# Optimization experiments

Measured on AMD Instinct MI355X. Metric: run time of the kernel, lower is better.

## Reference

```python
import jax, jax.numpy as jnp
import numpy as np

N_HEADS = 16
D_MODEL = 1024
D_HEAD = D_MODEL // N_HEADS


def setup_inputs() -> dict:
    key = jax.random.key(0)
    k1, k2, k3 = jax.random.split(key, 3)
    b, t, d = 2, 2048, D_MODEL
    x = jax.random.normal(k1, (b, t, d), dtype=jnp.float32)
    # Linear weights stored as [in, out] so y = x @ W (equivalent to torch's x @ W.T)
    w_qkv = jax.random.normal(k2, (d, 3 * d), dtype=jnp.float32) * (1.0 / np.sqrt(d))
    w_out = jax.random.normal(k3, (d, d), dtype=jnp.float32) * (1.0 / np.sqrt(d))
    return {"x": x, "w_qkv": w_qkv, "w_out": w_out}


def reference(x, w_qkv, w_out):
    b, t, d = x.shape
    h, dh = N_HEADS, D_HEAD
    qkv = x @ w_qkv                                   # (b, t, 3d)
    q, k, v = jnp.split(qkv, 3, axis=-1)
    # (b, h, t, dh)
    q = q.reshape(b, t, h, dh).transpose(0, 2, 1, 3)
    k = k.reshape(b, t, h, dh).transpose(0, 2, 1, 3)
    v = v.reshape(b, t, h, dh).transpose(0, 2, 1, 3)
    scale = 1.0 / np.sqrt(dh).astype(np.float32)
    att = jnp.einsum('bhqd,bhkd->bhqk', q, k) * scale  # (b, h, t, t)
    causal = jnp.tril(jnp.ones((t, t), dtype=bool))
    att = jnp.where(causal, att, -jnp.inf)
    att = jax.nn.softmax(att, axis=-1)
    y = jnp.einsum('bhqk,bhkd->bhqd', att, v)          # (b, h, t, dh)
    y = y.transpose(0, 2, 1, 3).reshape(b, t, d)
    return y @ w_out
```

## Files before the change

### kernel.cpp

```cpp
#include <hip/hip_runtime.h>
#include <hip/hip_bf16.h>
#include <stdint.h>

typedef __bf16 bf16x8 __attribute__((ext_vector_type(8)));
typedef float  f32x4  __attribute__((ext_vector_type(4)));

#define B_   2
#define T_   2048
#define H_   16
#define DH_  64
#define DM_  1024
#define BH_  (B_*H_)
#define M_   (B_*T_)

#define QSCALE 0.18033688f
#define FIXED_M 8.0f

static __device__ __forceinline__ void gload_lds16(const void* g, void* lds) {
  __builtin_amdgcn_global_load_lds(
      (const __attribute__((address_space(1))) void*)(uintptr_t)g,
      (__attribute__((address_space(3))) void*)(uint32_t)(uintptr_t)lds,
      16, 0, 0);
}

__global__ void k_prep(const float* __restrict__ x, const float* __restrict__ wqkv,
                       const float* __restrict__ wout, __hip_bfloat16* __restrict__ xb,
                       __hip_bfloat16* __restrict__ wqkvT, __hip_bfloat16* __restrict__ woutT) {
  __shared__ float tile[32][33];
  const int bid = blockIdx.x, tid = threadIdx.x;
  if (bid < 4096) {
    int i = bid * 256 + tid;
    float4 v = reinterpret_cast<const float4*>(x)[i];
    alignas(8) __hip_bfloat16 t[4] = {__float2bfloat16(v.x), __float2bfloat16(v.y),
                                      __float2bfloat16(v.z), __float2bfloat16(v.w)};
    reinterpret_cast<uint2*>(xb)[i] = *reinterpret_cast<const uint2*>(t);
    return;
  }
  const float* in; __hip_bfloat16* out; int K, N, n0, k0;
  if (bid < 7168) {
    int t = bid - 4096; in = wqkv; out = wqkvT; K = 1024; N = 3072;
    n0 = (t % 96) * 32; k0 = (t / 96) * 32;
  } else {
    int t = bid - 7168; in = wout; out = woutT; K = 1024; N = 1024;
    n0 = (t % 32) * 32; k0 = (t / 32) * 32;
  }
  int kl = tid >> 3, n4 = (tid & 7) * 4;
  float4 v = *reinterpret_cast<const float4*>(in + (size_t)(k0 + kl) * N + n0 + n4);
  tile[kl][n4 + 0] = v.x; tile[kl][n4 + 1] = v.y; tile[kl][n4 + 2] = v.z; tile[kl][n4 + 3] = v.w;
  __syncthreads();
  int nl = tid >> 3, k4 = (tid & 7) * 4;
  alignas(8) __hip_bfloat16 t[4];
  #pragma unroll
  for (int j = 0; j < 4; ++j) t[j] = __float2bfloat16(tile[k4 + j][nl]);
  *reinterpret_cast<uint2*>(out + (size_t)(n0 + nl) * K + k0 + k4) = *reinterpret_cast<const uint2*>(t);
}

template<int BM, int BN, int FM, int FN>
static __device__ __forceinline__ void gemm_core_pipe(
    const __hip_bfloat16* __restrict__ A, const __hip_bfloat16* __restrict__ BT,
    int K, int brow, int bcol, __hip_bfloat16* As, __hip_bfloat16* Bs,
    f32x4 acc[FM][FN]) {
  constexpr int WGN = BN / (16 * FN);
  constexpr int LOADS = BM / 64 + BN / 64;
  constexpr int ASLOT = BM * 32, BSLOT = BN * 32;
  const int tid = threadIdx.x, wave = tid >> 6, lane = tid & 63;
  const int wr = wave / WGN, wc = wave % WGN;
  const int llo = lane & 15, lhi = lane >> 4;
  const int nk = K / 32;
  const int schunk = (lane & 3) ^ ((lane >> 3) & 3);
  auto stage = [&](int ks, int slot) {
    #pragma unroll
    for (int c = wave; c < BM / 16; c += 4)
      gload_lds16(A + (size_t)(brow + c * 16 + (lane >> 2)) * K + ks * 32 + schunk * 8,
                  As + slot * ASLOT + c * 512);
    #pragma unroll
    for (int c = wave; c < BN / 16; c += 4)
      gload_lds16(BT + (size_t)(bcol + c * 16 + (lane >> 2)) * K + ks * 32 + schunk * 8,
                  Bs + slot * BSLOT + c * 512);
  };
  stage(0, 0);
  stage(1, 1);
  const int rchunk = lhi ^ ((llo >> 1) & 3);
  for (int ks = 0; ks < nk; ++ks) {
    if constexpr (LOADS == 4)      asm volatile("s_waitcnt vmcnt(4)" ::: "memory");
    else if constexpr (LOADS == 3) asm volatile("s_waitcnt vmcnt(3)" ::: "memory");
    else                           asm volatile("s_waitcnt vmcnt(0)" ::: "memory");
    __builtin_amdgcn_sched_barrier(0);
    __builtin_amdgcn_s_barrier();
    __builtin_amdgcn_sched_barrier(0);
    const int s2 = (ks + 2 < nk) ? ks + 2 : nk - 1;
    stage(s2, (ks + 2) % 3);
    const __hip_bfloat16* Asl = As + (ks % 3) * ASLOT;
    const __hip_bfloat16* Bsl = Bs + (ks % 3) * BSLOT;
    bf16x8 a[FM], b[FN];
    #pragma unroll
    for (int i = 0; i < FM; ++i)
      a[i] = *reinterpret_cast<const bf16x8*>(
          Asl + (wr * FM * 16 + i * 16 + llo) * 32 + rchunk * 8);
    #pragma unroll
    for (int j = 0; j < FN; ++j)
      b[j] = *reinterpret_cast<const bf16x8*>(
          Bsl + (wc * FN * 16 + j * 16 + llo) * 32 + rchunk * 8);
    __builtin_amdgcn_s_setprio(1);
    #pragma unroll
    for (int i = 0; i < FM; ++i)
      #pragma unroll
      for (int j = 0; j < FN; ++j)
        acc[i][j] = __builtin_amdgcn_mfma_f32_16x16x32_bf16(a[i], b[j], acc[i][j], 0, 0, 0);
    __builtin_amdgcn_s_setprio(0);
  }
  asm volatile("s_waitcnt vmcnt(0)" ::: "memory");
}

__global__ __launch_bounds__(256) void k_gemm_qkv(
    const __hip_bfloat16* __restrict__ A, const __hip_bfloat16* __restrict__ BT,
    __hip_bfloat16* __restrict__ q_ws, __hip_bfloat16* __restrict__ k_ws,
    __hip_bfloat16* __restrict__ vT) {
  alignas(16) __shared__ __hip_bfloat16 As[3 * 128 * 32];
  alignas(16) __shared__ __hip_bfloat16 Bs[3 * 128 * 32];
  f32x4 acc[4][4] = {};
  const int brow = blockIdx.y * 128, bcol = blockIdx.x * 128;
  gemm_core_pipe<128, 128, 4, 4>(A, BT, DM_, brow, bcol, As, Bs, acc);
  const int tid = threadIdx.x, wave = tid >> 6, lane = tid & 63;
  const int wr = wave >> 1, wc = wave & 1;
  const int llo = lane & 15, lhi = lane >> 4;
  #pragma unroll
  for (int i = 0; i < 4; ++i) {
    const int tbase = brow + wr * 64 + i * 16 + lhi * 4;
    const int b = tbase >> 11, t = tbase & 2047;
    #pragma unroll
    for (int j = 0; j < 4; ++j) {
      int n = bcol + wc * 64 + j * 16 + llo;
      int part = n >> 10, rem = n & 1023, hh = rem >> 6, dh = rem & 63;
      if (part == 2) {
        alignas(8) __hip_bfloat16 tv[4];
        #pragma unroll
        for (int r = 0; r < 4; ++r) tv[r] = __float2bfloat16(acc[i][j][r]);
        *reinterpret_cast<uint2*>(
            vT + (((size_t)(b * H_ + hh)) * DH_ + dh) * T_ + t) =
            *reinterpret_cast<const uint2*>(tv);
      } else {
        float sc = (part == 0) ? QSCALE : 1.0f;
        __hip_bfloat16* dst = (part == 0) ? q_ws : k_ws;
        #pragma unroll
        for (int r = 0; r < 4; ++r)
          dst[(((size_t)(b * H_ + hh)) * T_ + t + r) * DH_ + dh] =
              __float2bfloat16(acc[i][j][r] * sc);
      }
    }
  }
}

__global__ __launch_bounds__(256) void k_gemm_out(
    const __hip_bfloat16* __restrict__ A, const __hip_bfloat16* __restrict__ BT,
    float* __restrict__ C) {
  alignas(16) __shared__ __hip_bfloat16 As[3 * 128 * 32];
  alignas(16) __shared__ __hip_bfloat16 Bs[3 * 64 * 32];
  f32x4 acc[4][2] = {};
  const int brow = blockIdx.y * 128, bcol = blockIdx.x * 64;
  gemm_core_pipe<128, 64, 4, 2>(A, BT, DM_, brow, bcol, As, Bs, acc);
  const int tid = threadIdx.x, wave = tid >> 6, lane = tid & 63;
  const int wr = wave >> 1, wc = wave & 1;
  const int llo = lane & 15, lhi = lane >> 4;
  #pragma unroll
  for (int i = 0; i < 4; ++i)
    #pragma unroll
    for (int j = 0; j < 2; ++j) {
      int n = bcol + wc * 32 + j * 16 + llo;
      #pragma unroll
      for (int r = 0; r < 4; ++r) {
        int m = brow + wr * 64 + i * 16 + lhi * 4 + r;
        C[(size_t)m * DM_ + n] = acc[i][j][r];
      }
    }
}

__global__ __launch_bounds__(512) void k_attn(
    const __hip_bfloat16* __restrict__ Q, const __hip_bfloat16* __restrict__ Kk,
    const __hip_bfloat16* __restrict__ VT, __hip_bfloat16* __restrict__ Y) {
  alignas(16) __shared__ __hip_bfloat16 Ks[4][64 * 64];
  alignas(16) __shared__ __hip_bfloat16 Vs[4][64 * 64];
  alignas(16) __shared__ __hip_bfloat16 Ps[8][16 * 64];
  const int bh = blockIdx.y;
  const int p  = blockIdx.x;
  const int tid = threadIdx.x, wave = tid >> 6, lane = tid & 63;
  const int llo = lane & 15, lhi = lane >> 4;
  const int qt   = (wave < 4) ? (31 - p) : p;
  const int myNt = qt + 1;
  const int ntA  = 32 - p;
  const int q0 = qt * 64;
  const int qbase = q0 + (wave & 3) * 16;
  const int myq = qbase + llo;

  const __hip_bfloat16* kb = Kk + (size_t)bh * T_ * DH_;
  const __hip_bfloat16* vb = VT + (size_t)bh * DH_ * T_;

  const int srow = lane >> 3;
  const int schunk = (lane & 7) ^ srow;
  const int rb = wave * 8;

  bf16x8 aq[2];
  #pragma unroll
  for (int k0 = 0; k0 < 2; ++k0)
    aq[k0] = *reinterpret_cast<const bf16x8*>(
        Q + ((size_t)bh * T_ + myq) * DH_ + k0 * 32 + lhi * 8);

  float lsum = 0.f;
  f32x4 o[4] = {};

  gload_lds16(kb + (size_t)(rb + srow) * DH_ + schunk * 8, &Ks[0][rb * 64]);
  gload_lds16(vb + (size_t)(rb + srow) * T_ + schunk * 8, &Vs[0][rb * 64]);
  gload_lds16(kb + (size_t)(64 + rb + srow) * DH_ + schunk * 8, &Ks[1][rb * 64]);
  gload_lds16(vb + (size_t)(rb + srow) * T_ + 64 + schunk * 8, &Vs[1][rb * 64]);

  char* psw = reinterpret_cast<char*>(&Ps[wave][0]);

  for (int it = 0; it < ntA; ++it) {
    const int cur = it & 3;
    {
      const int ts = (it + 2 < ntA) ? (it + 2) : (ntA - 1);
      const int bs = (it + 2) & 3;
      const int tn = ts * 64;
      gload_lds16(kb + (size_t)(tn + rb + srow) * DH_ + schunk * 8, &Ks[bs][rb * 64]);
      gload_lds16(vb + (size_t)(rb + srow) * T_ + tn + schunk * 8, &Vs[bs][rb * 64]);
    }
    asm volatile("s_waitcnt vmcnt(4)" ::: "memory");
    __builtin_amdgcn_sched_barrier(0);
    __builtin_amdgcn_s_barrier();
    __builtin_amdgcn_sched_barrier(0);

    if (it < myNt) {
      const __hip_bfloat16* ksb = Ks[cur];
      const __hip_bfloat16* vsb = Vs[cur];

      f32x4 s[4];
      __builtin_amdgcn_s_setprio(1);
      #pragma unroll
      for (int jn = 0; jn < 4; ++jn) {
        const __hip_bfloat16* krow = ksb + (jn * 16 + llo) * 64;
        bf16x8 b0 = *reinterpret_cast<const bf16x8*>(krow + ((lhi ^ (llo & 7)) << 3));
        bf16x8 b1 = *reinterpret_cast<const bf16x8*>(krow + (((4 + lhi) ^ (llo & 7)) << 3));
        f32x4 z = {};
        z = __builtin_amdgcn_mfma_f32_16x16x32_bf16(b0, aq[0], z, 0, 0, 0);
        z = __builtin_amdgcn_mfma_f32_16x16x32_bf16(b1, aq[1], z, 0, 0, 0);
        s[jn] = z;
      }
      __builtin_amdgcn_s_setprio(0);
      if (it == myNt - 1) {
        #pragma unroll
        for (int jn = 0; jn < 4; ++jn)
          #pragma unroll
          for (int r = 0; r < 4; ++r) {
            int tprime = q0 + jn * 16 + lhi * 4 + r;
            if (tprime > myq) s[jn][r] = -INFINITY;
          }
      }
      #pragma unroll
      for (int jn = 0; jn < 4; ++jn) {
        float p0 = __builtin_amdgcn_exp2f(s[jn][0] - FIXED_M);
        float p1 = __builtin_amdgcn_exp2f(s[jn][1] - FIXED_M);
        float p2 = __builtin_amdgcn_exp2f(s[jn][2] - FIXED_M);
        float p3 = __builtin_amdgcn_exp2f(s[jn][3] - FIXED_M);
        lsum += (p0 + p1) + (p2 + p3);
        alignas(8) __hip_bfloat16 hp[4] = {
            __float2bfloat16(p0), __float2bfloat16(p1),
            __float2bfloat16(p2), __float2bfloat16(p3)};
        int wbyte = llo * 128 + ((((jn << 1) | (lhi >> 1)) ^ (llo & 7)) << 4) + ((lhi & 1) << 3);
        *reinterpret_cast<uint2*>(psw + wbyte) = *reinterpret_cast<const uint2*>(hp);
      }
      asm volatile("" ::: "memory");
      bf16x8 ap0 = *reinterpret_cast<const bf16x8*>(
          &Ps[wave][llo * 64 + ((lhi ^ (llo & 7)) << 3)]);
      bf16x8 ap1 = *reinterpret_cast<const bf16x8*>(
          &Ps[wave][llo * 64 + (((4 + lhi) ^ (llo & 7)) << 3)]);
      __builtin_amdgcn_s_setprio(1);
      #pragma unroll
      for (int jd = 0; jd < 4; ++jd) {
        const __hip_bfloat16* vrow = vsb + (jd * 16 + llo) * 64;
        bf16x8 v0 = *reinterpret_cast<const bf16x8*>(vrow + ((lhi ^ (llo & 7)) << 3));
        bf16x8 v1 = *reinterpret_cast<const bf16x8*>(vrow + (((4 + lhi) ^ (llo & 7)) << 3));
        o[jd] = __builtin_amdgcn_mfma_f32_16x16x32_bf16(v0, ap0, o[jd], 0, 0, 0);
        o[jd] = __builtin_amdgcn_mfma_f32_16x16x32_bf16(v1, ap1, o[jd], 0, 0, 0);
      }
      __builtin_amdgcn_s_setprio(0);
    }
  }

  lsum += __shfl_xor(lsum, 16);
  lsum += __shfl_xor(lsum, 32);
  const float inv = 1.0f / lsum;

  const int b = bh >> 4, h = bh & 15;
  __hip_bfloat16* yrow = Y + ((size_t)(b * T_ + myq)) * DM_ + h * 64;
  #pragma unroll
  for (int jd = 0; jd < 4; ++jd) {
    alignas(8) __hip_bfloat16 t4[4];
    #pragma unroll
    for (int r = 0; r < 4; ++r) t4[r] = __float2bfloat16(o[jd][r] * inv);
    *reinterpret_cast<uint2*>(yrow + jd * 16 + lhi * 4) =
        *reinterpret_cast<const uint2*>(t4);
  }
}

extern "C" void kernel_launch(void* const* d_in, const int* in_sizes, int n_in,
                              void* d_out, int out_size, void* d_ws, size_t ws_size,
                              hipStream_t stream) {
  const float* x     = (const float*)d_in[0];
  const float* w_qkv = (const float*)d_in[1];
  const float* w_out = (const float*)d_in[2];
  float* out = (float*)d_out;
  char* ws = (char*)d_ws;

  size_t off = 0;
  __hip_bfloat16* xb    = (__hip_bfloat16*)(ws + off); off += (size_t)M_ * DM_ * 2;
  __hip_bfloat16* wqkvT = (__hip_bfloat16*)(ws + off); off += (size_t)3 * DM_ * DM_ * 2;
  __hip_bfloat16* woutT = (__hip_bfloat16*)(ws + off); off += (size_t)DM_ * DM_ * 2;
  __hip_bfloat16* q_ws  = (__hip_bfloat16*)(ws + off); off += (size_t)M_ * DM_ * 2;
  __hip_bfloat16* k_ws  = (__hip_bfloat16*)(ws + off); off += (size_t)M_ * DM_ * 2;
  __hip_bfloat16* vT    = (__hip_bfloat16*)(ws + off); off += (size_t)M_ * DM_ * 2;
  __hip_bfloat16* y_ws  = (__hip_bfloat16*)(ws + off); off += (size_t)M_ * DM_ * 2;
  (void)ws_size; (void)in_sizes; (void)n_in; (void)out_size;

  k_prep<<<8192, 256, 0, stream>>>(x, w_qkv, w_out, xb, wqkvT, woutT);

  k_gemm_qkv<<<dim3(3 * DM_ / 128, M_ / 128), 256, 0, stream>>>(xb, wqkvT, q_ws, k_ws, vT);

  k_attn<<<dim3(T_ / 128, BH_), 512, 0, stream>>>(q_ws, k_ws, vT, y_ws);

  k_gemm_out<<<dim3(DM_ / 64, M_ / 128), 256, 0, stream>>>(y_ws, woutT, out);
}
```

Before: 99.88 us.

## Rewrite QKV GEMM with 256x256 tiles, 8 waves, and double-buffered K=64 stages

Replaces the 128x128, 4-wave triple-buffered QKV projection GEMM with a 256x256 tile computed by 8 waves (512 threads). Each K step is 64 wide, double-buffered in LDS with an XOR swizzle, and split into four sub-phases that interleave the next-tile loads with MFMA work. The goal is more reuse per LDS byte and fewer global loads per FLOP. In exchange it uses 128 KB of LDS per block, adds extra barriers per sub-phase, and launches only 192 blocks, which may underfill the GPU's compute units.

```diff
diff --git a/kernel.cpp b/kernel.cpp
--- a/kernel.cpp
+++ b/kernel.cpp
@@ -15,6 +15,8 @@
 
 #define QSCALE 0.18033688f
 #define FIXED_M 8.0f
+
+#define SBAR() __builtin_amdgcn_sched_barrier(0)
 
 static __device__ __forceinline__ void gload_lds16(const void* g, void* lds) {
   __builtin_amdgcn_global_load_lds(
@@ -85,9 +87,9 @@
     if constexpr (LOADS == 4)      asm volatile("s_waitcnt vmcnt(4)" ::: "memory");
     else if constexpr (LOADS == 3) asm volatile("s_waitcnt vmcnt(3)" ::: "memory");
     else                           asm volatile("s_waitcnt vmcnt(0)" ::: "memory");
-    __builtin_amdgcn_sched_barrier(0);
+    SBAR();
     __builtin_amdgcn_s_barrier();
-    __builtin_amdgcn_sched_barrier(0);
+    SBAR();
     const int s2 = (ks + 2 < nk) ? ks + 2 : nk - 1;
     stage(s2, (ks + 2) % 3);
     const __hip_bfloat16* Asl = As + (ks % 3) * ASLOT;
@@ -112,25 +114,97 @@
   asm volatile("s_waitcnt vmcnt(0)" ::: "memory");
 }
 
-__global__ __launch_bounds__(256) void k_gemm_qkv(
+__global__ __launch_bounds__(512) void k_gemm_qkv(
     const __hip_bfloat16* __restrict__ A, const __hip_bfloat16* __restrict__ BT,
     __hip_bfloat16* __restrict__ q_ws, __hip_bfloat16* __restrict__ k_ws,
     __hip_bfloat16* __restrict__ vT) {
-  alignas(16) __shared__ __hip_bfloat16 As[3 * 128 * 32];
-  alignas(16) __shared__ __hip_bfloat16 Bs[3 * 128 * 32];
-  f32x4 acc[4][4] = {};
-  const int brow = blockIdx.y * 128, bcol = blockIdx.x * 128;
-  gemm_core_pipe<128, 128, 4, 4>(A, BT, DM_, brow, bcol, As, Bs, acc);
+  alignas(16) __shared__ __hip_bfloat16 Adb[2][256 * 64];
+  alignas(16) __shared__ __hip_bfloat16 Bdb[2][256 * 64];
   const int tid = threadIdx.x, wave = tid >> 6, lane = tid & 63;
-  const int wr = wave >> 1, wc = wave & 1;
   const int llo = lane & 15, lhi = lane >> 4;
+  const int wr = wave >> 2, wcn = wave & 3;
+  const int bcol = blockIdx.x * 256, brow = blockIdx.y * 256;
+
+  f32x4 acc[8][4] = {};
+
+  auto stageHalf = [&](const __hip_bfloat16* P, int baseRow, int ktS, int half,
+                       __hip_bfloat16* tile) {
+    #pragma unroll
+    for (int l = 0; l < 2; ++l) {
+      const int idxb = l * 512 + wave * 64;
+      const int rowt = half * 128 + (idxb >> 3) + (lane >> 3);
+      const int ch = lane & 7;
+      gload_lds16(P + (size_t)(baseRow + rowt) * DM_ + ktS * 64 + ((ch ^ (rowt & 7)) * 8),
+                  tile + half * (128 * 64) + idxb * 8);
+    }
+  };
+
+  stageHalf(A, brow, 0, 0, Adb[0]);
+  stageHalf(A, brow, 0, 1, Adb[0]);
+  stageHalf(BT, bcol, 0, 0, Bdb[0]);
+  stageHalf(BT, bcol, 0, 1, Bdb[0]);
+
+  for (int kt = 0; kt < 16; ++kt) {
+    const int buf = kt & 1;
+    const int bufn = buf ^ 1;
+    const int ktn = (kt < 15) ? kt + 1 : 15;
+    const __hip_bfloat16* At = Adb[buf];
+    const __hip_bfloat16* Bt = Bdb[buf];
+    #pragma unroll
+    for (int p = 0; p < 4; ++p) {
+      if (p == 0) {
+        stageHalf(A, brow, ktn, 0, Adb[bufn]);
+        stageHalf(A, brow, ktn, 1, Adb[bufn]);
+        asm volatile("s_waitcnt vmcnt(4)" ::: "memory");
+      } else if (p == 1) {
+        stageHalf(BT, bcol, ktn, 0, Bdb[bufn]);
+        stageHalf(BT, bcol, ktn, 1, Bdb[bufn]);
+      }
+      SBAR();
+      __builtin_amdgcn_s_barrier();
+      SBAR();
+      const int i0 = p >> 1, j0 = p & 1;
+      bf16x8 af[4][2], bfr[2][2];
+      #pragma unroll
+      for (int ii = 0; ii < 4; ++ii) {
+        const int rowt = wr * 128 + (i0 * 4 + ii) * 16 + llo;
+        #pragma unroll
+        for (int kk = 0; kk < 2; ++kk)
+          af[ii][kk] = *reinterpret_cast<const bf16x8*>(
+              At + rowt * 64 + (((kk * 4 + lhi) ^ (rowt & 7)) * 8));
+      }
+      #pragma unroll
+      for (int j2 = 0; j2 < 2; ++j2) {
+        const int rowb = wcn * 64 + (j0 * 2 + j2) * 16 + llo;
+        #pragma unroll
+        for (int kk = 0; kk < 2; ++kk)
+          bfr[j2][kk] = *reinterpret_cast<const bf16x8*>(
+              Bt + rowb * 64 + (((kk * 4 + lhi) ^ (rowb & 7)) * 8));
+      }
+      __builtin_amdgcn_s_setprio(1);
+      #pragma unroll
+      for (int ii = 0; ii < 4; ++ii)
+        #pragma unroll
+        for (int j2 = 0; j2 < 2; ++j2)
+          #pragma unroll
+          for (int kk = 0; kk < 2; ++kk)
+            acc[i0 * 4 + ii][j0 * 2 + j2] = __builtin_amdgcn_mfma_f32_16x16x32_bf16(
+                af[ii][kk], bfr[j2][kk], acc[i0 * 4 + ii][j0 * 2 + j2], 0, 0, 0);
+      __builtin_amdgcn_s_setprio(0);
+      SBAR();
+      __builtin_amdgcn_s_barrier();
+      SBAR();
+    }
+  }
+  asm volatile("s_waitcnt vmcnt(0)" ::: "memory");
+
   #pragma unroll
-  for (int i = 0; i < 4; ++i) {
-    const int tbase = brow + wr * 64 + i * 16 + lhi * 4;
+  for (int i = 0; i < 8; ++i) {
+    const int tbase = brow + wr * 128 + i * 16 + lhi * 4;
     const int b = tbase >> 11, t = tbase & 2047;
     #pragma unroll
     for (int j = 0; j < 4; ++j) {
-      int n = bcol + wc * 64 + j * 16 + llo;
+      int n = bcol + wcn * 64 + j * 16 + llo;
       int part = n >> 10, rem = n & 1023, hh = rem >> 6, dh = rem & 63;
       if (part == 2) {
         alignas(8) __hip_bfloat16 tv[4];
@@ -225,9 +299,9 @@
       gload_lds16(vb + (size_t)(rb + srow) * T_ + tn + schunk * 8, &Vs[bs][rb * 64]);
     }
     asm volatile("s_waitcnt vmcnt(4)" ::: "memory");
-    __builtin_amdgcn_sched_barrier(0);
+    SBAR();
     __builtin_amdgcn_s_barrier();
-    __builtin_amdgcn_sched_barrier(0);
+    SBAR();
 
     if (it < myNt) {
       const __hip_bfloat16* ksb = Ks[cur];
@@ -323,7 +397,7 @@
 
   k_prep<<<8192, 256, 0, stream>>>(x, w_qkv, w_out, xb, wqkvT, woutT);
 
-  k_gemm_qkv<<<dim3(3 * DM_ / 128, M_ / 128), 256, 0, stream>>>(xb, wqkvT, q_ws, k_ws, vT);
+  k_gemm_qkv<<<dim3(3 * DM_ / 256, M_ / 256), 512, 0, stream>>>(xb, wqkvT, q_ws, k_ws, vT);
 
   k_attn<<<dim3(T_ / 128, BH_), 512, 0, stream>>>(q_ws, k_ws, vT, y_ws);
 
```

After: 104.9 us. 5.0% more time.
